# Performance work log

Measured on AMD Instinct MI355X. Metric: run time of the kernel, lower is better.

The kernel has to match this reference:

```python
import jax, jax.numpy as jnp
import numpy as np

PARTICLE_RADIUS = 0.025
RADIUS_SCALE = 1.5
EXTENT = 6.0 * RADIUS_SCALE * PARTICLE_RADIUS   # 0.225
RADIUS = 0.5 * EXTENT                           # 0.1125 search radius
N_FLUID, N_WALL, K = 16000, 8000, 64
KS = 4  # kernel size per axis


def _radius_neighbors(pin, pout, radius, k, exclude_self=False):
    n = pout.shape[0]
    idx = np.zeros((n, k), np.int32)
    mask = np.zeros((n, k), bool)
    r2 = radius * radius
    for s in range(0, n, 2048):
        q = pout[s:s + 2048]
        d2 = ((q[:, None, :] - pin[None, :, :]) ** 2).sum(-1)
        within = d2 < r2
        if exclude_self:
            within &= d2 > 1e-18
        for i in range(q.shape[0]):
            js = np.flatnonzero(within[i])[:k]
            idx[s + i, :js.size] = js
            mask[s + i, :js.size] = True
    return idx, mask


def setup_inputs():
    rng = np.random.RandomState(0)
    L = (N_FLUID / 6700.0) ** (1.0 / 3.0)  # box side -> ~40 nbrs in RADIUS
    fluid_pos = (rng.rand(N_FLUID, 3) * L).astype(np.float32)
    wall_pos = np.stack([rng.rand(N_WALL) * L, -0.3 * rng.rand(N_WALL), rng.rand(N_WALL) * L], -1).astype(np.float32)
    fluid_vel = (0.5 * rng.randn(N_FLUID, 3)).astype(np.float32)
    nv = rng.randn(N_WALL, 3)
    wall_normal_vec = (nv / np.linalg.norm(nv, axis=1, keepdims=True)).astype(np.float32)
    nbr_wf, mask_wf = _radius_neighbors(wall_pos, fluid_pos, RADIUS, K)
    nbr_ff, mask_ff = _radius_neighbors(fluid_pos, fluid_pos, RADIUS, K, exclude_self=True)
    def cw(ci, co):
        return (rng.randn(KS, KS, KS, ci, co) / np.sqrt(ci * KS ** 3)).astype(np.float32)
    def dw(ci, co):
        return (rng.randn(ci, co) / np.sqrt(ci)).astype(np.float32)
    def bias(co):
        return (0.01 * rng.randn(co)).astype(np.float32)
    inp = dict(fluid_pos=fluid_pos, wall_pos=wall_pos, fluid_vel=fluid_vel, wall_normal_vec=wall_normal_vec,
               nbr_wf=nbr_wf, mask_wf=mask_wf, nbr_ff=nbr_ff, mask_ff=mask_ff,
               W_wall1=cw(3, 32), b_wall1=bias(32), W_fluid1=cw(3, 32), b_fluid1=bias(32),
               W_d1=dw(3, 32), b_d1=bias(32),
               W_c2=cw(96, 64), b_c2=bias(64), W_d2=dw(96, 64), b_d2=bias(64),
               W_c3=cw(64, 64), b_c3=bias(64), W_d3=dw(64, 64), b_d3=bias(64),
               W_c4=cw(64, 3), b_c4=bias(3), W_d4=dw(64, 3), b_d4=bias(3))
    return {k_: jnp.asarray(v) for k_, v in inp.items()}


def _ball_to_cube(p):
    """Volume-preserving ball->cylinder->cube map (Open3D coordinate_mapping)."""
    eps = 1e-12
    x, y, z = p[..., 0], p[..., 1], p[..., 2]
    sq = x * x + y * y + z * z
    norm = jnp.sqrt(jnp.maximum(sq, eps))
    rho = jnp.sqrt(jnp.maximum(x * x + y * y, eps))
    top = 1.25 * z * z > x * x + y * y
    s_top = jnp.sqrt(3.0 * norm / (norm + jnp.abs(z)))
    xs = jnp.where(top, x * s_top, x * norm / rho)
    ys = jnp.where(top, y * s_top, y * norm / rho)
    zs = jnp.where(top, jnp.sign(z) * norm, 1.5 * z)
    degen = sq < eps
    xs = jnp.where(degen, 0.0, xs)
    ys = jnp.where(degen, 0.0, ys)
    zs = jnp.where(degen, 0.0, zs)
    # cylinder -> cube: area-preserving disc->square on (x, y)
    rxy = jnp.sqrt(jnp.maximum(xs * xs + ys * ys, eps))
    use_x = jnp.abs(ys) <= jnp.abs(xs)
    dx = jnp.where(use_x & (jnp.abs(xs) > eps), xs, 1.0)
    dy = jnp.where((~use_x) & (jnp.abs(ys) > eps), ys, 1.0)
    c = 4.0 / jnp.pi
    xc = jnp.where(use_x, jnp.sign(xs) * rxy, jnp.sign(ys) * rxy * c * jnp.arctan(xs / dy))
    yc = jnp.where(use_x, jnp.sign(xs) * rxy * c * jnp.arctan(ys / dx), jnp.sign(ys) * rxy)
    deg2 = (xs * xs + ys * ys) < eps
    xc = jnp.where(deg2, 0.0, xc)
    yc = jnp.where(deg2, 0.0, yc)
    return jnp.stack([xc, yc, zs], -1)


def _cconv(feat, pos_in, pos_out, nbr, mask, W, b):
    """ContinuousConv: trilinear kernel interp, poly6 window, normalize=False."""
    n, k = nbr.shape
    cin, cout = W.shape[3], W.shape[4]
    d = (pos_in[nbr] - pos_out[:, None, :]) / RADIUS          # [n,k,3] in unit ball
    d = jnp.where(mask[..., None], d, 0.0)
    r2 = jnp.sum(d * d, -1)
    win = jnp.clip((1.0 - r2) ** 3, 0.0, 1.0)                  # poly6 window
    u = _ball_to_cube(d)                                       # [-1,1]^3
    c = jnp.clip((u * 0.5 + 0.5) * (KS - 1), 0.0, KS - 1.0)   # align_corners coords
    i0 = jnp.clip(jnp.floor(c), 0.0, KS - 2.0)
    f = c - i0
    i0 = i0.astype(jnp.int32)
    feats = feat[nbr] * jnp.where(mask, win, 0.0)[..., None]   # [n,k,cin]
    A = jnp.zeros((n, KS ** 3, cin), feat.dtype)               # per-cell accumulators
    rows = jnp.arange(n)[:, None]
    for cx in (0, 1):
        wx = f[..., 0] if cx else 1.0 - f[..., 0]
        for cy in (0, 1):
            wy = f[..., 1] if cy else 1.0 - f[..., 1]
            for cz in (0, 1):
                wz = f[..., 2] if cz else 1.0 - f[..., 2]
                cell = ((i0[..., 0] + cx) * KS + (i0[..., 1] + cy)) * KS + (i0[..., 2] + cz)
                A = A.at[rows, cell].add((wx * wy * wz)[..., None] * feats)
    return jnp.einsum('nfc,fcd->nd', A, W.reshape(KS ** 3, cin, cout)) + b


def _forward(fluid_pos, wall_pos, fluid_vel, wall_normal_vec, nbr_wf, mask_wf, nbr_ff, mask_ff,
             W_wall1, b_wall1, W_fluid1, b_fluid1, W_d1, b_d1, W_c2, b_c2, W_d2, b_d2,
             W_c3, b_c3, W_d3, b_d3, W_c4, b_c4, W_d4, b_d4):
    wall_1 = jax.nn.relu(_cconv(wall_normal_vec, wall_pos, fluid_pos, nbr_wf, mask_wf, W_wall1, b_wall1))
    fluid_1 = jax.nn.relu(_cconv(fluid_vel, fluid_pos, fluid_pos, nbr_ff, mask_ff, W_fluid1, b_fluid1))
    dense_1 = fluid_vel @ W_d1 + b_d1
    out_1 = jnp.concatenate([wall_1, fluid_1, dense_1], -1)    # [N,96]
    out_2 = jax.nn.relu(_cconv(out_1, fluid_pos, fluid_pos, nbr_ff, mask_ff, W_c2, b_c2) + out_1 @ W_d2 + b_d2)
    out_3 = jax.nn.relu(out_2 + _cconv(out_2, fluid_pos, fluid_pos, nbr_ff, mask_ff, W_c3, b_c3) + out_2 @ W_d3 + b_d3)
    return _cconv(out_3, fluid_pos, fluid_pos, nbr_ff, mask_ff, W_c4, b_c4) + out_3 @ W_d4 + b_d4


def reference(fluid_pos, wall_pos, fluid_vel, wall_normal_vec, nbr_wf, mask_wf, nbr_ff, mask_ff,
              W_wall1, b_wall1, W_fluid1, b_fluid1, W_d1, b_d1, W_c2, b_c2, W_d2, b_d2,
              W_c3, b_c3, W_d3, b_d3, W_c4, b_c4, W_d4, b_d4):
    return _forward(fluid_pos, wall_pos, fluid_vel, wall_normal_vec, nbr_wf, mask_wf, nbr_ff, mask_ff,
                    W_wall1, b_wall1, W_fluid1, b_fluid1, W_d1, b_d1, W_c2, b_c2, W_d2, b_d2,
                    W_c3, b_c3, W_d3, b_d3, W_c4, b_c4, W_d4, b_d4)
```

## Files before the change

### kernel.cpp

```cpp
#include <hip/hip_runtime.h>
#include <hip/hip_bf16.h>


#define M_FLUID 16000
#define KNBR 64

typedef __attribute__((ext_vector_type(8))) short bf16x8;
typedef __attribute__((ext_vector_type(4))) float f32x4;
typedef __attribute__((ext_vector_type(4))) unsigned short u16x4;

__device__ __forceinline__ ushort f2bf(float f) {
    __hip_bfloat16 h = __float2bfloat16(f);
    return *(ushort*)&h;
}

__device__ __forceinline__ float sgnf(float v) {
    return (v > 0.f) ? 1.f : ((v < 0.f) ? -1.f : 0.f);
}

__device__ __forceinline__ void ball_to_cube(float x, float y, float z,
                                             float& xc, float& yc, float& zc) {
    const float eps = 1e-12f;
    float sq  = x*x + y*y + z*z;
    float nrm = sqrtf(fmaxf(sq, eps));
    float rho = sqrtf(fmaxf(x*x + y*y, eps));
    bool  top = (1.25f*z*z > x*x + y*y);
    float s_top = sqrtf(3.0f*nrm/(nrm + fabsf(z)));
    float xs = top ? x*s_top : x*nrm/rho;
    float ys = top ? y*s_top : y*nrm/rho;
    float zs = top ? sgnf(z)*nrm : 1.5f*z;
    if (sq < eps) { xs = 0.f; ys = 0.f; zs = 0.f; }
    float rxy = sqrtf(fmaxf(xs*xs + ys*ys, eps));
    bool use_x = fabsf(ys) <= fabsf(xs);
    float dx = (use_x && fabsf(xs) > eps) ? xs : 1.0f;
    float dy = (!use_x && fabsf(ys) > eps) ? ys : 1.0f;
    const float c4pi = 1.2732395447351628f;
    float xc_, yc_;
    if (use_x) {
        xc_ = sgnf(xs)*rxy;
        yc_ = sgnf(xs)*rxy*c4pi*atanf(ys/dx);
    } else {
        xc_ = sgnf(ys)*rxy*c4pi*atanf(xs/dy);
        yc_ = sgnf(ys)*rxy;
    }
    if (xs*xs + ys*ys < eps) { xc_ = 0.f; yc_ = 0.f; }
    xc = xc_; yc = yc_; zc = zs;
}

__global__ void geom_dual_kernel(const float* __restrict__ fluid_pos,
                                 const float* __restrict__ wall_pos,
                                 const int*  __restrict__ nbrF,
                                 const int*  __restrict__ nbrW,
                                 float4* __restrict__ gFf, int* __restrict__ gIf,
                                 float4* __restrict__ gFw, int* __restrict__ gIw,
                                 int M) {
    int t = blockIdx.x * blockDim.x + threadIdx.x;
    if (t >= M * KNBR) return;
    const float* pos_in; const int* nbr; float4* geomF; int* geomI; int excl_self;
    if (blockIdx.y == 0) { pos_in = fluid_pos; nbr = nbrF; geomF = gFf; geomI = gIf; excl_self = 1; }
    else                 { pos_in = wall_pos;  nbr = nbrW; geomF = gFw; geomI = gIw; excl_self = 0; }
    int n = t >> 6;
    int k = t & 63;
    int j = nbr[t];
    float px = fluid_pos[n*3+0], py = fluid_pos[n*3+1], pz = fluid_pos[n*3+2];
    float qx = pos_in[(size_t)j*3+0], qy = pos_in[(size_t)j*3+1], qz = pos_in[(size_t)j*3+2];
    float dx = qx - px, dy = qy - py, dz = qz - pz;

    bool valid;
    if (k == 0) {
#pragma clang fp contract(off)
        float d2f = dx*dx + dy*dy;
        d2f = d2f + dz*dz;
        double d2 = (double)d2f;
        const double RADIUS_D = 0.5*(6.0*1.5*0.025);
        valid = d2 < RADIUS_D*RADIUS_D;
        if (excl_self) valid = valid && (d2 > 1e-18);
    } else {
        valid = (j != 0);
    }

    const float Rf = (float)(0.5*(6.0*1.5*0.025));
    float ux = dx / Rf, uy = dy / Rf, uz = dz / Rf;
    float r2 = ux*ux + uy*uy; r2 += uz*uz;
    float w1 = 1.f - r2;
    float win = fminf(fmaxf(w1*w1*w1, 0.f), 1.f);

    float bx, by, bz;
    ball_to_cube(ux, uy, uz, bx, by, bz);
    float cx = fminf(fmaxf((bx*0.5f + 0.5f)*3.f, 0.f), 3.f);
    float cy = fminf(fmaxf((by*0.5f + 0.5f)*3.f, 0.f), 3.f);
    float cz = fminf(fmaxf((bz*0.5f + 0.5f)*3.f, 0.f), 3.f);
    float ix = fminf(fmaxf(floorf(cx), 0.f), 2.f);
    float iy = fminf(fmaxf(floorf(cy), 0.f), 2.f);
    float iz = fminf(fmaxf(floorf(cz), 0.f), 2.f);
    float fx = cx - ix, fy = cy - iy, fz = cz - iz;
    int cell = ((int)ix*4 + (int)iy)*4 + (int)iz;

    geomF[t] = make_float4(valid ? win : 0.f, fx, fy, fz);
    geomI[t] = cell;
}

template<int CIN>
__global__ __launch_bounds__(64) void abuild_s_kernel(
        const float* __restrict__ feat,
        const int*   __restrict__ nbr,
        const float4* __restrict__ geomF,
        const int*   __restrict__ geomI,
        const float* __restrict__ dense,
        ushort* __restrict__ A,
        int m0, int m1, int Ktot) {
    constexpr int SP = 72;
    constexpr int NT = CIN / 16;
    __shared__ ushort S[64*SP];
    __shared__ ushort FW[CIN*SP];
    int l = threadIdx.x;
    int n = m0 + blockIdx.x;
    if (n >= m1) return;

    {
        uint4 z = make_uint4(0,0,0,0);
        uint4* Sv = (uint4*)S;
#pragma unroll
        for (int i = 0; i < (64*SP*2)/(16*64); ++i)
            Sv[l + 64*i] = z;
    }
    size_t t = (size_t)n * KNBR + l;
    float4 g = geomF[t];
    int cell = geomI[t];
    int j = nbr[t];
    {
        float win = g.x;
        float x1 = g.y, y1 = g.z, z1 = g.w;
        float x0 = 1.f-x1, y0 = 1.f-y1, z0 = 1.f-z1;
        float w00 = y0*z0*win, w01 = y0*z1*win, w10 = y1*z0*win, w11 = y1*z1*win;
        ushort* Sc = S + cell*SP + l;
        Sc[0*SP]  = f2bf(x0*w00);
        Sc[1*SP]  = f2bf(x0*w01);
        Sc[4*SP]  = f2bf(x0*w10);
        Sc[5*SP]  = f2bf(x0*w11);
        Sc[16*SP] = f2bf(x1*w00);
        Sc[17*SP] = f2bf(x1*w01);
        Sc[20*SP] = f2bf(x1*w10);
        Sc[21*SP] = f2bf(x1*w11);
    }
    {
        const float* frow = feat + (size_t)j * CIN;
#pragma unroll
        for (int c4 = 0; c4 < CIN; c4 += 4) {
            float4 v = *(const float4*)(frow + c4);
            FW[(c4+0)*SP + l] = f2bf(v.x);
            FW[(c4+1)*SP + l] = f2bf(v.y);
            FW[(c4+2)*SP + l] = f2bf(v.z);
            FW[(c4+3)*SP + l] = f2bf(v.w);
        }
    }
    int lm = l & 15, koct = l >> 4;
    f32x4 acc[4][NT];
#pragma unroll
    for (int mt = 0; mt < 4; ++mt)
#pragma unroll
        for (int nt = 0; nt < NT; ++nt)
            acc[mt][nt] = (f32x4){0.f, 0.f, 0.f, 0.f};
#pragma unroll
    for (int ks = 0; ks < 2; ++ks) {
        bf16x8 sf[4];
#pragma unroll
        for (int mt = 0; mt < 4; ++mt)
            sf[mt] = *(const bf16x8*)&S[(mt*16 + lm)*SP + ks*32 + koct*8];
#pragma unroll
        for (int nt = 0; nt < NT; ++nt) {
            bf16x8 ff = *(const bf16x8*)&FW[(nt*16 + lm)*SP + ks*32 + koct*8];
#pragma unroll
            for (int mt = 0; mt < 4; ++mt)
                acc[mt][nt] = __builtin_amdgcn_mfma_f32_16x16x32_bf16(
                                  sf[mt], ff, acc[mt][nt], 0, 0, 0);
        }
    }
    ushort* AT = FW;
#pragma unroll
    for (int nt = 0; nt < NT; ++nt)
#pragma unroll
        for (int mt = 0; mt < 4; ++mt) {
            u16x4 pk;
            pk.x = f2bf(acc[mt][nt][0]);
            pk.y = f2bf(acc[mt][nt][1]);
            pk.z = f2bf(acc[mt][nt][2]);
            pk.w = f2bf(acc[mt][nt][3]);
            *(u16x4*)&AT[(nt*16 + lm)*SP + mt*16 + koct*4] = pk;
        }
    ushort* Arow = A + (size_t)(n - m0) * Ktot;
#pragma unroll
    for (int it = 0; it < CIN/8; ++it) {
        int i = l + 64*it;
        int ch = i >> 3, cc = (i & 7) * 8;
        uint4 v = *(const uint4*)&AT[ch*SP + cc];
        *(uint4*)&Arow[(ch << 6) + cc] = v;
    }
#pragma unroll
    for (int c0 = 0; c0 < CIN; c0 += 64) {
        int ch = c0 + l;
        if (ch < CIN) Arow[64*CIN + ch] = f2bf(dense[(size_t)n*CIN + ch]);
    }
}

__global__ __launch_bounds__(64) void abuild_s3_dual_kernel(
        const float* __restrict__ featW, const float* __restrict__ featF,
        const int*   __restrict__ nbrW,  const int*   __restrict__ nbrF,
        const float4* __restrict__ gFw,  const int* __restrict__ gIw,
        const float4* __restrict__ gFf,  const int* __restrict__ gIf,
        ushort* __restrict__ A0, ushort* __restrict__ A1, int M) {
    constexpr int SP = 72;
    constexpr int Ktot = 192;
    __shared__ ushort S[64*SP];
    __shared__ ushort FW[16*SP];
    const float* feat; const int* nbr; const float4* geomF; const int* geomI; ushort* A;
    if (blockIdx.y == 0) { feat = featW; nbr = nbrW; geomF = gFw; geomI = gIw; A = A0; }
    else                 { feat = featF; nbr = nbrF; geomF = gFf; geomI = gIf; A = A1; }
    int l = threadIdx.x;
    int n = blockIdx.x;
    if (n >= M) return;

    {
        uint4 z = make_uint4(0,0,0,0);
        uint4* Sv = (uint4*)S;
#pragma unroll
        for (int i = 0; i < 9; ++i) Sv[l + 64*i] = z;
        uint4* Fv = (uint4*)FW;
#pragma unroll
        for (int i = 0; i < 3; ++i) {
            int idx = l + 64*i;
            if (idx < (16*SP*2)/16) Fv[idx] = z;
        }
    }
    size_t t = (size_t)n * KNBR + l;
    float4 g = geomF[t];
    int cell = geomI[t];
    int j = nbr[t];
    {
        float win = g.x;
        float x1 = g.y, y1 = g.z, z1 = g.w;
        float x0 = 1.f-x1, y0 = 1.f-y1, z0 = 1.f-z1;
        float w00 = y0*z0*win, w01 = y0*z1*win, w10 = y1*z0*win, w11 = y1*z1*win;
        ushort* Sc = S + cell*SP + l;
        Sc[0*SP]  = f2bf(x0*w00);
        Sc[1*SP]  = f2bf(x0*w01);
        Sc[4*SP]  = f2bf(x0*w10);
        Sc[5*SP]  = f2bf(x0*w11);
        Sc[16*SP] = f2bf(x1*w00);
        Sc[17*SP] = f2bf(x1*w01);
        Sc[20*SP] = f2bf(x1*w10);
        Sc[21*SP] = f2bf(x1*w11);
    }
    {
        const float* fr = feat + (size_t)j * 3;
        FW[0*SP + l] = f2bf(fr[0]);
        FW[1*SP + l] = f2bf(fr[1]);
        FW[2*SP + l] = f2bf(fr[2]);
    }
    int lm = l & 15, koct = l >> 4;
    f32x4 acc[4];
#pragma unroll
    for (int mt = 0; mt < 4; ++mt) acc[mt] = (f32x4){0.f,0.f,0.f,0.f};
#pragma unroll
    for (int ks = 0; ks < 2; ++ks) {
        bf16x8 ff = *(const bf16x8*)&FW[lm*SP + ks*32 + koct*8];
#pragma unroll
        for (int mt = 0; mt < 4; ++mt) {
            bf16x8 sf = *(const bf16x8*)&S[(mt*16 + lm)*SP + ks*32 + koct*8];
            acc[mt] = __builtin_amdgcn_mfma_f32_16x16x32_bf16(sf, ff, acc[mt], 0, 0, 0);
        }
    }
    ushort* AT = FW;
    if (lm < 3) {
#pragma unroll
        for (int mt = 0; mt < 4; ++mt) {
            u16x4 pk;
            pk.x = f2bf(acc[mt][0]);
            pk.y = f2bf(acc[mt][1]);
            pk.z = f2bf(acc[mt][2]);
            pk.w = f2bf(acc[mt][3]);
            *(u16x4*)&AT[lm*SP + mt*16 + koct*4] = pk;
        }
    }
    ushort* Arow = A + (size_t)n * Ktot;
    if (l < 24) {
        int ch = l >> 3, cc = (l & 7) * 8;
        *(uint4*)&Arow[ch*64 + cc] = *(const uint4*)&AT[ch*SP + cc];
    }
}

__global__ void dense1_kernel(const float* __restrict__ vel,
                              const float* __restrict__ Wd,
                              const float* __restrict__ bd,
                              float* __restrict__ out1, int M) {
    int t = blockIdx.x * blockDim.x + threadIdx.x;
    if (t >= M*32) return;
    int n = t >> 5, c = t & 31;
    float v = bd[c] + vel[n*3+0]*Wd[c] + vel[n*3+1]*Wd[32+c] + vel[n*3+2]*Wd[64+c];
    out1[(size_t)n*96 + 64 + c] = v;
}

__device__ __forceinline__ void wprep_one(const float* Wc, int Kc,
                                          const float* Wd, int N,
                                          ushort* Wt, int Ktot, int t) {
    int nn = t / Ktot, k = t - nn * Ktot;
    float v;
    if (k < Kc) {
        int cinl = Kc >> 6;
        int ch = k >> 6, cl = k & 63;
        v = Wc[(size_t)(cl*cinl + ch)*N + nn];
    } else {
        v = Wd[(size_t)(k-Kc)*N + nn];
    }
    Wt[(size_t)nn*Ktot + k] = f2bf(v);
}

__global__ void wprep_all_kernel(
        const float* __restrict__ W_wall1, const float* __restrict__ W_fluid1,
        const float* __restrict__ W_c2, const float* __restrict__ W_d2,
        const float* __restrict__ W_c3, const float* __restrict__ W_d3,
        const float* __restrict__ W_c4,
        ushort* __restrict__ Wt1a, ushort* __restrict__ Wt1b,
        ushort* __restrict__ Wt2, ushort* __restrict__ Wt3,
        ushort* __restrict__ Wt4) {
    int t = blockIdx.x * 256 + threadIdx.x;
    const int s0 = 32*192, s1 = s0 + 32*192, s2 = s1 + 64*6240,
              s3 = s2 + 64*4160, s4 = s3 + 192*64;
    if (t < s0) {
        wprep_one(W_wall1, 192, nullptr, 32, Wt1a, 192, t);
    } else if (t < s1) {
        wprep_one(W_fluid1, 192, nullptr, 32, Wt1b, 192, t - s0);
    } else if (t < s2) {
        wprep_one(W_c2, 6144, W_d2, 64, Wt2, 6240, t - s1);
    } else if (t < s3) {
        wprep_one(W_c3, 4096, W_d3, 64, Wt3, 4160, t - s2);
    } else if (t < s4) {
        int u = t - s3;
        int row = u >> 6, ch = u & 63;
        int cell = row / 3, c = row - cell*3;
        Wt4[row*64 + ch] = f2bf(W_c4[(cell*64 + ch)*3 + c]);
    }
}

__global__ __launch_bounds__(256) void gemm_l1_kernel(
        const ushort* __restrict__ A0, const ushort* __restrict__ A1,
        const ushort* __restrict__ Wt0, const ushort* __restrict__ Wt1,
        const float* __restrict__ b0, const float* __restrict__ b1,
        float* __restrict__ out1, int M) {
    constexpr int Ktot = 192, nks = 6, NCT = 2;
    const ushort* A;  const ushort* Wt; const float* bias; int ocol;
    if (blockIdx.y == 0) { A = A0; Wt = Wt0; bias = b0; ocol = 0; }
    else                 { A = A1; Wt = Wt1; bias = b1; ocol = 32; }
    int tid = threadIdx.x;
    int w = tid >> 6, l = tid & 63;
    int lm = l & 15, koct = l >> 4;
    int mb = blockIdx.x;

    const ushort* Arow = A + (size_t)(mb*64 + w*16 + lm) * Ktot + koct*8;
    const ushort* Wrow = Wt + (size_t)lm * Ktot + koct*8;

    f32x4 acc[NCT];
#pragma unroll
    for (int ct = 0; ct < NCT; ++ct) acc[ct] = (f32x4){0.f,0.f,0.f,0.f};

    bf16x8 ac = *(const bf16x8*)(Arow);
    bf16x8 bc[NCT];
#pragma unroll
    for (int ct = 0; ct < NCT; ++ct)
        bc[ct] = *(const bf16x8*)(Wrow + (size_t)ct*16*Ktot);
#pragma unroll
    for (int ks = 0; ks < nks; ++ks) {
        bf16x8 an = {};
        bf16x8 bn[NCT] = {};
        if (ks + 1 < nks) {
            int k0 = (ks + 1) * 32;
            an = *(const bf16x8*)(Arow + k0);
#pragma unroll
            for (int ct = 0; ct < NCT; ++ct)
                bn[ct] = *(const bf16x8*)(Wrow + (size_t)ct*16*Ktot + k0);
        }
#pragma unroll
        for (int ct = 0; ct < NCT; ++ct)
            acc[ct] = __builtin_amdgcn_mfma_f32_16x16x32_bf16(ac, bc[ct], acc[ct], 0, 0, 0);
        ac = an;
#pragma unroll
        for (int ct = 0; ct < NCT; ++ct) bc[ct] = bn[ct];
    }

    int rbase = mb*64 + w*16 + koct*4;
#pragma unroll
    for (int ct = 0; ct < NCT; ++ct) {
        int col = ct*16 + lm;
        float bb = bias[col];
#pragma unroll
        for (int r = 0; r < 4; ++r) {
            float v = fmaxf(acc[ct][r] + bb, 0.f);
            out1[(size_t)(rbase + r)*96 + ocol + col] = v;
        }
    }
}

__global__ __launch_bounds__(256) void gemm7_kernel(
        const ushort* __restrict__ A, int Ktot,
        const ushort* __restrict__ Wt,
        float* __restrict__ Cpart, int rows, int nks, int KS) {
    constexpr int N = 64;
    constexpr int SP = 40;
    __shared__ ushort Ash[2][128][SP];
    __shared__ ushort Bsh[2][64][SP];
    int tid = threadIdx.x;
    int w = tid >> 6, l = tid & 63;
    int lm = l & 15, koct = l >> 4;
    int mb = blockIdx.x;
    int per = (nks + KS - 1) / KS;
    int ksa = blockIdx.y * per;
    int ksb = ksa + per; if (ksb > nks) ksb = nks;
    int nk = ksb - ksa;

    f32x4 acc[2][4];
#pragma unroll
    for (int fi = 0; fi < 2; ++fi)
#pragma unroll
        for (int nt = 0; nt < 4; ++nt) acc[fi][nt] = (f32x4){0.f,0.f,0.f,0.f};

    int rS  = tid >> 2;
    int kb4 = tid & 3;
    int rA0 = mb*128 + rS;       if (rA0 >= rows) rA0 = rows - 1;
    int rA1 = mb*128 + rS + 64;  if (rA1 >= rows) rA1 = rows - 1;

    bf16x8 ra0, ra1, rb;
    auto load_regs = [&](int ks) {
        int kk = ks*32 + kb4*8;
        ra0 = *(const bf16x8*)&A[(size_t)rA0*Ktot + kk];
        ra1 = *(const bf16x8*)&A[(size_t)rA1*Ktot + kk];
        rb  = *(const bf16x8*)&Wt[(size_t)rS*Ktot + kk];
    };
    auto store_lds = [&](int buf) {
        *(bf16x8*)&Ash[buf][rS][kb4*8]      = ra0;
        *(bf16x8*)&Ash[buf][rS + 64][kb4*8] = ra1;
        *(bf16x8*)&Bsh[buf][rS][kb4*8]      = rb;
    };

    if (nk > 0) {
        load_regs(ksa);
        store_lds(0);
        __syncthreads();
        for (int i = 0; i < nk; ++i) {
            int buf = i & 1;
            bool nxt = (i + 1 < nk);
            if (nxt) load_regs(ksa + i + 1);
            bf16x8 a0 = *(const bf16x8*)&Ash[buf][w*32 + lm][koct*8];
            bf16x8 a1 = *(const bf16x8*)&Ash[buf][w*32 + 16 + lm][koct*8];
#pragma unroll
            for (int nt = 0; nt < 4; ++nt) {
                bf16x8 b = *(const bf16x8*)&Bsh[buf][nt*16 + lm][koct*8];
                acc[0][nt] = __builtin_amdgcn_mfma_f32_16x16x32_bf16(a0, b, acc[0][nt], 0, 0, 0);
                acc[1][nt] = __builtin_amdgcn_mfma_f32_16x16x32_bf16(a1, b, acc[1][nt], 0, 0, 0);
            }
            if (nxt) {
                store_lds(buf ^ 1);
                __syncthreads();
            }
        }
    }

    float* Cp = Cpart + ((size_t)blockIdx.y * rows + mb*128 + w*32) * N;
    int gr0 = mb*128 + w*32;
#pragma unroll
    for (int fi = 0; fi < 2; ++fi)
#pragma unroll
        for (int nt = 0; nt < 4; ++nt)
#pragma unroll
            for (int r = 0; r < 4; ++r) {
                int row = fi*16 + koct*4 + r;
                if (gr0 + row < rows)
                    Cp[row * N + nt*16 + lm] = acc[fi][nt][r];
            }
}

__global__ __launch_bounds__(256) void reduce_kernel(
        const float* __restrict__ Cpart, int rows, int N, int KS,
        const float* __restrict__ b1, const float* __restrict__ b2,
        const float* __restrict__ res,
        float* __restrict__ out, int ostride, int ocol, int m_base, int relu,
        ushort* __restrict__ outb) {
    int idx = blockIdx.x * 256 + threadIdx.x;
    int nq = N >> 2;
    if (idx >= rows * nq) return;
    int row = idx / nq;
    int c4 = (idx - row * nq) * 4;
    size_t slab = (size_t)rows * N;
    const float* p = Cpart + (size_t)row * N + c4;
    float s0 = 0.f, s1 = 0.f, s2 = 0.f, s3 = 0.f;
    for (int k = 0; k < KS; ++k) {
        float4 v = *(const float4*)(p + slab * k);
        s0 += v.x; s1 += v.y; s2 += v.z; s3 += v.w;
    }
    s0 += b1[c4+0]; s1 += b1[c4+1]; s2 += b1[c4+2]; s3 += b1[c4+3];
    if (b2) { s0 += b2[c4+0]; s1 += b2[c4+1]; s2 += b2[c4+2]; s3 += b2[c4+3]; }
    if (res) {
        const float* rr = res + (size_t)(m_base + row) * 64 + c4;
        s0 += rr[0]; s1 += rr[1]; s2 += rr[2]; s3 += rr[3];
    }
    if (relu) {
        s0 = fmaxf(s0, 0.f); s1 = fmaxf(s1, 0.f);
        s2 = fmaxf(s2, 0.f); s3 = fmaxf(s3, 0.f);
    }
    float* o = out + (size_t)(m_base + row) * ostride + ocol + c4;
    *(float4*)o = make_float4(s0, s1, s2, s3);
    if (outb) {
        u16x4 pk;
        pk.x = f2bf(s0); pk.y = f2bf(s1); pk.z = f2bf(s2); pk.w = f2bf(s3);
        *(u16x4*)&outb[(size_t)(m_base + row) * 64 + c4] = pk;
    }
}

__global__ __launch_bounds__(256) void g4_mfma_kernel(
        const ushort* __restrict__ out3b,
        const ushort* __restrict__ Wt4,
        float* __restrict__ G, int M) {
    constexpr int SP = 72;
    __shared__ ushort Bsh[192*SP];
    int tid = threadIdx.x;
    for (int u = tid; u < 192*8; u += 256) {
        int row = u >> 3, seg = u & 7;
        *(bf16x8*)&Bsh[row*SP + seg*8] = *(const bf16x8*)&Wt4[row*64 + seg*8];
    }
    __syncthreads();
    int w = tid >> 6, l = tid & 63;
    int lm = l & 15, koct = l >> 4;
    int row0 = blockIdx.x*64 + w*16;
    const ushort* Arow = out3b + (size_t)(row0 + lm)*64 + koct*8;
    bf16x8 a0 = *(const bf16x8*)(Arow);
    bf16x8 a1 = *(const bf16x8*)(Arow + 32);
    f32x4 acc[12];
#pragma unroll
    for (int nt = 0; nt < 12; ++nt) acc[nt] = (f32x4){0.f,0.f,0.f,0.f};
#pragma unroll
    for (int nt = 0; nt < 12; ++nt) {
        bf16x8 b = *(const bf16x8*)&Bsh[(nt*16 + lm)*SP + koct*8];
        acc[nt] = __builtin_amdgcn_mfma_f32_16x16x32_bf16(a0, b, acc[nt], 0, 0, 0);
    }
#pragma unroll
    for (int nt = 0; nt < 12; ++nt) {
        bf16x8 b = *(const bf16x8*)&Bsh[(nt*16 + lm)*SP + 32 + koct*8];
        acc[nt] = __builtin_amdgcn_mfma_f32_16x16x32_bf16(a1, b, acc[nt], 0, 0, 0);
    }
#pragma unroll
    for (int nt = 0; nt < 12; ++nt)
#pragma unroll
        for (int r = 0; r < 4; ++r)
            G[(size_t)(row0 + koct*4 + r)*192 + nt*16 + lm] = acc[nt][r];
}

__global__ __launch_bounds__(256) void l4_scatter_kernel(
        const float* __restrict__ G,
        const float4* __restrict__ geomF,
        const int*   __restrict__ geomI,
        const int*   __restrict__ nbr,
        const float* __restrict__ out3,
        const float* __restrict__ Wd4,
        const float* __restrict__ b_c4, const float* __restrict__ b_d4,
        float* __restrict__ out, int M) {
    __shared__ float Wsh[192];
    int tid = threadIdx.x;
    if (tid < 192) Wsh[tid] = Wd4[tid];
    __syncthreads();
    int wv = tid >> 6, l = tid & 63;
    int n = blockIdx.x*4 + wv;
    if (n >= M) return;
    size_t t = (size_t)n * KNBR + l;
    float4 g = geomF[t];
    int cell = geomI[t];
    int j = nbr[t];
    float a0 = 0.f, a1 = 0.f, a2 = 0.f;
    float win = g.x;
    if (win > 0.f) {
        float x1 = g.y, y1 = g.z, z1 = g.w;
        float x0 = 1.f-x1, y0 = 1.f-y1, z0 = 1.f-z1;
        float w[8] = {x0*y0*z0, x0*y0*z1, x0*y1*z0, x0*y1*z1,
                      x1*y0*z0, x1*y0*z1, x1*y1*z0, x1*y1*z1};
        const int co[8] = {0,1,4,5,16,17,20,21};
        const float* Gj = G + (size_t)j*192;
#pragma unroll
        for (int i = 0; i < 8; ++i) {
            const float* Gc = Gj + (cell + co[i])*3;
            float ww = win * w[i];
            a0 += ww*Gc[0]; a1 += ww*Gc[1]; a2 += ww*Gc[2];
        }
    }
    {
        float v = out3[(size_t)n*64 + l];
        a0 += v*Wsh[l*3+0]; a1 += v*Wsh[l*3+1]; a2 += v*Wsh[l*3+2];
    }
#pragma unroll
    for (int off = 32; off; off >>= 1) {
        a0 += __shfl_down(a0, off, 64);
        a1 += __shfl_down(a1, off, 64);
        a2 += __shfl_down(a2, off, 64);
    }
    if (l == 0) {
        out[n*3+0] = a0 + b_c4[0] + b_d4[0];
        out[n*3+1] = a1 + b_c4[1] + b_d4[1];
        out[n*3+2] = a2 + b_c4[2] + b_d4[2];
    }
}

extern "C" void kernel_launch(void* const* d_in, const int* in_sizes, int n_in,
                              void* d_out, int out_size, void* d_ws, size_t ws_size,
                              hipStream_t stream) {
    const float* fluid_pos = (const float*)d_in[0];
    const float* wall_pos  = (const float*)d_in[1];
    const float* fluid_vel = (const float*)d_in[2];
    const float* wall_nrm  = (const float*)d_in[3];
    const int*   nbr_wf    = (const int*)d_in[4];
    const int*   nbr_ff    = (const int*)d_in[6];
    const float* W_wall1   = (const float*)d_in[8];
    const float* b_wall1   = (const float*)d_in[9];
    const float* W_fluid1  = (const float*)d_in[10];
    const float* b_fluid1  = (const float*)d_in[11];
    const float* W_d1      = (const float*)d_in[12];
    const float* b_d1      = (const float*)d_in[13];
    const float* W_c2      = (const float*)d_in[14];
    const float* b_c2      = (const float*)d_in[15];
    const float* W_d2      = (const float*)d_in[16];
    const float* b_d2      = (const float*)d_in[17];
    const float* W_c3      = (const float*)d_in[18];
    const float* b_c3      = (const float*)d_in[19];
    const float* W_d3      = (const float*)d_in[20];
    const float* b_d3      = (const float*)d_in[21];
    const float* W_c4      = (const float*)d_in[22];
    const float* b_c4      = (const float*)d_in[23];
    const float* W_d4      = (const float*)d_in[24];
    const float* b_d4      = (const float*)d_in[25];

    const int M = M_FLUID;
    char* ws = (char*)d_ws;
    size_t off = 0;
    auto carve = [&](size_t bytes) {
        char* p = ws + off;
        off = (off + bytes + 255) & ~(size_t)255;
        return p;
    };
    float4* gF_ff = (float4*)carve((size_t)M*KNBR*sizeof(float4));
    int*    gI_ff = (int*)   carve((size_t)M*KNBR*4);
    float4* gF_wf = (float4*)carve((size_t)M*KNBR*sizeof(float4));
    int*    gI_wf = (int*)   carve((size_t)M*KNBR*4);
    float*  out1  = (float*) carve((size_t)M*96*4);
    float*  out2  = (float*) carve((size_t)M*64*4);
    float*  out3  = (float*) carve((size_t)M*64*4);
    ushort* out3b = (ushort*)carve((size_t)M*64*2);
    float*  Gbuf  = (float*) carve((size_t)M*192*4);
    ushort* Wt1a  = (ushort*)carve((size_t)32*192*2);
    ushort* Wt1b  = (ushort*)carve((size_t)32*192*2);
    ushort* Wt2   = (ushort*)carve((size_t)64*6240*2);
    ushort* Wt3   = (ushort*)carve((size_t)64*4160*2);
    ushort* Wt4   = (ushort*)carve((size_t)192*64*2);
    float*  Cpart = (float*) carve((size_t)8*M*64*4);
    ushort* Abuf  = (ushort*)(ws + off);
    size_t availA = (ws_size > off) ? (ws_size - off) : 0;

    auto chunkR = [&](int Ktot) -> int {
        size_t r = availA / ((size_t)Ktot * 2);
        if (r > (size_t)M) r = (size_t)M;
        r &= ~(size_t)127;
        if (r < 128) r = 128;
        return (int)r;
    };

    {
        int total = 2*32*192 + 64*6240 + 64*4160 + 192*64;
        wprep_all_kernel<<<(total + 255)/256, 256, 0, stream>>>(
            W_wall1, W_fluid1, W_c2, W_d2, W_c3, W_d3, W_c4,
            Wt1a, Wt1b, Wt2, Wt3, Wt4);
    }
    {
        int total = M * KNBR, thr = 256;
        geom_dual_kernel<<<dim3((total + thr - 1)/thr, 2), thr, 0, stream>>>(
            fluid_pos, wall_pos, nbr_ff, nbr_wf, gF_ff, gI_ff, gF_wf, gI_wf, M);
    }
    dense1_kernel<<<(M*32 + 255)/256, 256, 0, stream>>>(fluid_vel, W_d1, b_d1, out1, M);

    {
        ushort* A0 = Abuf;
        ushort* A1 = Abuf + (size_t)M*192;
        abuild_s3_dual_kernel<<<dim3(M, 2), 64, 0, stream>>>(
            wall_nrm, fluid_vel, nbr_wf, nbr_ff,
            gF_wf, gI_wf, gF_ff, gI_ff, A0, A1, M);
        gemm_l1_kernel<<<dim3(M/64, 2), 256, 0, stream>>>(
            A0, A1, Wt1a, Wt1b, b_wall1, b_fluid1, out1, M);
    }
    {
        int Ktot = 6240, nks = 195, KS = 8, R = chunkR(Ktot);
        for (int m0 = 0; m0 < M; m0 += R) {
            int rows = (M - m0 < R) ? (M - m0) : R;
            abuild_s_kernel<96><<<rows, 64, 0, stream>>>(
                out1, nbr_ff, gF_ff, gI_ff, out1, Abuf, m0, m0+rows, Ktot);
            gemm7_kernel<<<dim3((rows+127)/128, KS), 256, 0, stream>>>(
                Abuf, Ktot, Wt2, Cpart, rows, nks, KS);
            reduce_kernel<<<(rows*16 + 255)/256, 256, 0, stream>>>(
                Cpart, rows, 64, KS, b_c2, b_d2, nullptr,
                out2, 64, 0, m0, 1, nullptr);
        }
    }
    {
        int Ktot = 4160, nks = 130, KS = 8, R = chunkR(Ktot);
        for (int m0 = 0; m0 < M; m0 += R) {
            int rows = (M - m0 < R) ? (M - m0) : R;
            abuild_s_kernel<64><<<rows, 64, 0, stream>>>(
                out2, nbr_ff, gF_ff, gI_ff, out2, Abuf, m0, m0+rows, Ktot);
            gemm7_kernel<<<dim3((rows+127)/128, KS), 256, 0, stream>>>(
                Abuf, Ktot, Wt3, Cpart, rows, nks, KS);
            reduce_kernel<<<(rows*16 + 255)/256, 256, 0, stream>>>(
                Cpart, rows, 64, KS, b_c3, b_d3, out2,
                out3, 64, 0, m0, 1, out3b);
        }
    }
    g4_mfma_kernel<<<M/64, 256, 0, stream>>>(out3b, Wt4, Gbuf, M);
    l4_scatter_kernel<<<(M+3)/4, 256, 0, stream>>>(
        Gbuf, gF_ff, gI_ff, nbr_ff, out3, W_d4, b_c4, b_d4, (float*)d_out, M);
}
```

Baseline: 386.3 us.

## Software-pipeline A-matrix build and GEMM across chunks in fused launches

Merges the neighbor-feature A-build and the split-K GEMM into one kernel launch whose blocks run either role. Chunk c's A-build now runs concurrently with chunk c-1's GEMM, using double-buffered A storage. The A-build packs four neighbourhoods per 256-thread block and processes channels in two halves to cut shared memory. Cpart is indexed globally so a single reduce runs at the end. The cost is a fixed chunk size of 4000 rows, which assumes the workspace holds two A buffers, plus mixed-role blocks competing for resources.

Result: slower. 433.4 us (+12.2%).

```diff
diff --git a/kernel.cpp b/kernel.cpp
--- a/kernel.cpp
+++ b/kernel.cpp
@@ -101,28 +101,25 @@
 }
 
 template<int CIN>
-__global__ __launch_bounds__(64) void abuild_s_kernel(
-        const float* __restrict__ feat,
-        const int*   __restrict__ nbr,
-        const float4* __restrict__ geomF,
-        const int*   __restrict__ geomI,
-        const float* __restrict__ dense,
-        ushort* __restrict__ A,
+__device__ __forceinline__ void abuild_body(char* smem, int blk,
+        const float* __restrict__ feat, const int* __restrict__ nbr,
+        const float4* __restrict__ geomF, const int* __restrict__ geomI,
+        const float* __restrict__ dense, ushort* __restrict__ A,
         int m0, int m1, int Ktot) {
+    constexpr int H = CIN / 2;
+    constexpr int NTH = H / 16;
     constexpr int SP = 72;
-    constexpr int NT = CIN / 16;
-    __shared__ ushort S[64*SP];
-    __shared__ ushort FW[CIN*SP];
-    int l = threadIdx.x;
-    int n = m0 + blockIdx.x;
+    int w = threadIdx.x >> 6, l = threadIdx.x & 63;
+    ushort* S  = (ushort*)(smem + (size_t)w * ((64 + H) * SP * 2));
+    ushort* FW = S + 64*SP;
+    int n = m0 + blk*4 + w;
     if (n >= m1) return;
 
     {
         uint4 z = make_uint4(0,0,0,0);
         uint4* Sv = (uint4*)S;
 #pragma unroll
-        for (int i = 0; i < (64*SP*2)/(16*64); ++i)
-            Sv[l + 64*i] = z;
+        for (int i = 0; i < 9; ++i) Sv[l + 64*i] = z;
     }
     size_t t = (size_t)n * KNBR + l;
     float4 g = geomF[t];
@@ -143,63 +140,158 @@
         Sc[20*SP] = f2bf(x1*w10);
         Sc[21*SP] = f2bf(x1*w11);
     }
-    {
-        const float* frow = feat + (size_t)j * CIN;
-#pragma unroll
-        for (int c4 = 0; c4 < CIN; c4 += 4) {
-            float4 v = *(const float4*)(frow + c4);
+    int lm = l & 15, koct = l >> 4;
+    const float* frow = feat + (size_t)j * CIN;
+    ushort* Arow = A + (size_t)(n - m0) * Ktot;
+#pragma unroll
+    for (int h = 0; h < 2; ++h) {
+#pragma unroll
+        for (int c4 = 0; c4 < H; c4 += 4) {
+            float4 v = *(const float4*)(frow + h*H + c4);
             FW[(c4+0)*SP + l] = f2bf(v.x);
             FW[(c4+1)*SP + l] = f2bf(v.y);
             FW[(c4+2)*SP + l] = f2bf(v.z);
             FW[(c4+3)*SP + l] = f2bf(v.w);
         }
-    }
-    int lm = l & 15, koct = l >> 4;
-    f32x4 acc[4][NT];
-#pragma unroll
-    for (int mt = 0; mt < 4; ++mt)
-#pragma unroll
-        for (int nt = 0; nt < NT; ++nt)
-            acc[mt][nt] = (f32x4){0.f, 0.f, 0.f, 0.f};
-#pragma unroll
-    for (int ks = 0; ks < 2; ++ks) {
-        bf16x8 sf[4];
+        f32x4 acc[4][NTH];
 #pragma unroll
         for (int mt = 0; mt < 4; ++mt)
-            sf[mt] = *(const bf16x8*)&S[(mt*16 + lm)*SP + ks*32 + koct*8];
-#pragma unroll
-        for (int nt = 0; nt < NT; ++nt) {
-            bf16x8 ff = *(const bf16x8*)&FW[(nt*16 + lm)*SP + ks*32 + koct*8];
+#pragma unroll
+            for (int nt = 0; nt < NTH; ++nt)
+                acc[mt][nt] = (f32x4){0.f,0.f,0.f,0.f};
+#pragma unroll
+        for (int ks = 0; ks < 2; ++ks) {
+            bf16x8 sf[4];
 #pragma unroll
             for (int mt = 0; mt < 4; ++mt)
-                acc[mt][nt] = __builtin_amdgcn_mfma_f32_16x16x32_bf16(
-                                  sf[mt], ff, acc[mt][nt], 0, 0, 0);
-        }
-    }
-    ushort* AT = FW;
-#pragma unroll
-    for (int nt = 0; nt < NT; ++nt)
-#pragma unroll
-        for (int mt = 0; mt < 4; ++mt) {
-            u16x4 pk;
-            pk.x = f2bf(acc[mt][nt][0]);
-            pk.y = f2bf(acc[mt][nt][1]);
-            pk.z = f2bf(acc[mt][nt][2]);
-            pk.w = f2bf(acc[mt][nt][3]);
-            *(u16x4*)&AT[(nt*16 + lm)*SP + mt*16 + koct*4] = pk;
-        }
-    ushort* Arow = A + (size_t)(n - m0) * Ktot;
-#pragma unroll
-    for (int it = 0; it < CIN/8; ++it) {
-        int i = l + 64*it;
-        int ch = i >> 3, cc = (i & 7) * 8;
-        uint4 v = *(const uint4*)&AT[ch*SP + cc];
-        *(uint4*)&Arow[(ch << 6) + cc] = v;
+                sf[mt] = *(const bf16x8*)&S[(mt*16 + lm)*SP + ks*32 + koct*8];
+#pragma unroll
+            for (int nt = 0; nt < NTH; ++nt) {
+                bf16x8 ff = *(const bf16x8*)&FW[(nt*16 + lm)*SP + ks*32 + koct*8];
+#pragma unroll
+                for (int mt = 0; mt < 4; ++mt)
+                    acc[mt][nt] = __builtin_amdgcn_mfma_f32_16x16x32_bf16(
+                                      sf[mt], ff, acc[mt][nt], 0, 0, 0);
+            }
+        }
+        ushort* AT = FW;
+#pragma unroll
+        for (int nt = 0; nt < NTH; ++nt)
+#pragma unroll
+            for (int mt = 0; mt < 4; ++mt) {
+                u16x4 pk;
+                pk.x = f2bf(acc[mt][nt][0]);
+                pk.y = f2bf(acc[mt][nt][1]);
+                pk.z = f2bf(acc[mt][nt][2]);
+                pk.w = f2bf(acc[mt][nt][3]);
+                *(u16x4*)&AT[(nt*16 + lm)*SP + mt*16 + koct*4] = pk;
+            }
+#pragma unroll
+        for (int it = 0; it < H/8; ++it) {
+            int i = l + 64*it;
+            int ch = i >> 3, cc = (i & 7) * 8;
+            *(uint4*)&Arow[(h*H + ch)*64 + cc] = *(const uint4*)&AT[ch*SP + cc];
+        }
     }
 #pragma unroll
     for (int c0 = 0; c0 < CIN; c0 += 64) {
         int ch = c0 + l;
         if (ch < CIN) Arow[64*CIN + ch] = f2bf(dense[(size_t)n*CIN + ch]);
+    }
+}
+
+__device__ __forceinline__ void gemm_body(char* smem, int gblk,
+        const ushort* __restrict__ A, int Ktot, const ushort* __restrict__ Wt,
+        float* __restrict__ Cpart, int rows, int gm0, int nks, int KS, int Mtot) {
+    constexpr int SP = 40;
+    ushort* Ash = (ushort*)smem;
+    ushort* Bsh = Ash + 2*128*SP;
+    int tid = threadIdx.x;
+    int w = tid >> 6, l = tid & 63;
+    int lm = l & 15, koct = l >> 4;
+    int mb = gblk / KS;
+    int ksy = gblk - mb*KS;
+    int per = (nks + KS - 1) / KS;
+    int ksa = ksy * per;
+    int ksb = ksa + per; if (ksb > nks) ksb = nks;
+    int nk = ksb - ksa;
+
+    f32x4 acc[2][4];
+#pragma unroll
+    for (int fi = 0; fi < 2; ++fi)
+#pragma unroll
+        for (int nt = 0; nt < 4; ++nt) acc[fi][nt] = (f32x4){0.f,0.f,0.f,0.f};
+
+    int rS  = tid >> 2;
+    int kb4 = tid & 3;
+    int rA0 = mb*128 + rS;       if (rA0 >= rows) rA0 = rows - 1;
+    int rA1 = mb*128 + rS + 64;  if (rA1 >= rows) rA1 = rows - 1;
+
+    bf16x8 ra0, ra1, rb;
+    auto load_regs = [&](int ks) {
+        int kk = ks*32 + kb4*8;
+        ra0 = *(const bf16x8*)&A[(size_t)rA0*Ktot + kk];
+        ra1 = *(const bf16x8*)&A[(size_t)rA1*Ktot + kk];
+        rb  = *(const bf16x8*)&Wt[(size_t)rS*Ktot + kk];
+    };
+    auto store_lds = [&](int buf) {
+        *(bf16x8*)&Ash[(buf*128 + rS)*SP + kb4*8]      = ra0;
+        *(bf16x8*)&Ash[(buf*128 + rS + 64)*SP + kb4*8] = ra1;
+        *(bf16x8*)&Bsh[(buf*64 + rS)*SP + kb4*8]       = rb;
+    };
+
+    if (nk > 0) {
+        load_regs(ksa);
+        store_lds(0);
+        __syncthreads();
+        for (int i = 0; i < nk; ++i) {
+            int buf = i & 1;
+            bool nxt = (i + 1 < nk);
+            if (nxt) load_regs(ksa + i + 1);
+            bf16x8 a0 = *(const bf16x8*)&Ash[(buf*128 + w*32 + lm)*SP + koct*8];
+            bf16x8 a1 = *(const bf16x8*)&Ash[(buf*128 + w*32 + 16 + lm)*SP + koct*8];
+#pragma unroll
+            for (int nt = 0; nt < 4; ++nt) {
+                bf16x8 b = *(const bf16x8*)&Bsh[(buf*64 + nt*16 + lm)*SP + koct*8];
+                acc[0][nt] = __builtin_amdgcn_mfma_f32_16x16x32_bf16(a0, b, acc[0][nt], 0, 0, 0);
+                acc[1][nt] = __builtin_amdgcn_mfma_f32_16x16x32_bf16(a1, b, acc[1][nt], 0, 0, 0);
+            }
+            if (nxt) {
+                store_lds(buf ^ 1);
+                __syncthreads();
+            }
+        }
+    }
+
+    float* Cp = Cpart + ((size_t)ksy * Mtot + gm0 + mb*128 + w*32) * 64;
+    int gr0 = mb*128 + w*32;
+#pragma unroll
+    for (int fi = 0; fi < 2; ++fi)
+#pragma unroll
+        for (int nt = 0; nt < 4; ++nt)
+#pragma unroll
+            for (int r = 0; r < 4; ++r) {
+                int row = fi*16 + koct*4 + r;
+                if (gr0 + row < rows)
+                    Cp[row * 64 + nt*16 + lm] = acc[fi][nt][r];
+            }
+}
+
+template<int CIN>
+__global__ __launch_bounds__(256) void fused_stage_kernel(
+        const ushort* __restrict__ Ag, int Ktot, const ushort* __restrict__ Wt,
+        float* __restrict__ Cpart, int grows, int ggm0, int nks, int KS,
+        int Mtot, int G_gemm,
+        const float* __restrict__ feat, const int* __restrict__ nbr,
+        const float4* __restrict__ geomF, const int* __restrict__ geomI,
+        const float* __restrict__ dense, ushort* __restrict__ Aa,
+        int am0, int am1) {
+    extern __shared__ char smem[];
+    if ((int)blockIdx.x < G_gemm) {
+        gemm_body(smem, blockIdx.x, Ag, Ktot, Wt, Cpart, grows, ggm0, nks, KS, Mtot);
+    } else {
+        abuild_body<CIN>(smem, blockIdx.x - G_gemm, feat, nbr, geomF, geomI,
+                         dense, Aa, am0, am1, Ktot);
     }
 }
 
@@ -398,84 +490,6 @@
             out1[(size_t)(rbase + r)*96 + ocol + col] = v;
         }
     }
-}
-
-__global__ __launch_bounds__(256) void gemm7_kernel(
-        const ushort* __restrict__ A, int Ktot,
-        const ushort* __restrict__ Wt,
-        float* __restrict__ Cpart, int rows, int nks, int KS) {
-    constexpr int N = 64;
-    constexpr int SP = 40;
-    __shared__ ushort Ash[2][128][SP];
-    __shared__ ushort Bsh[2][64][SP];
-    int tid = threadIdx.x;
-    int w = tid >> 6, l = tid & 63;
-    int lm = l & 15, koct = l >> 4;
-    int mb = blockIdx.x;
-    int per = (nks + KS - 1) / KS;
-    int ksa = blockIdx.y * per;
-    int ksb = ksa + per; if (ksb > nks) ksb = nks;
-    int nk = ksb - ksa;
-
-    f32x4 acc[2][4];
-#pragma unroll
-    for (int fi = 0; fi < 2; ++fi)
-#pragma unroll
-        for (int nt = 0; nt < 4; ++nt) acc[fi][nt] = (f32x4){0.f,0.f,0.f,0.f};
-
-    int rS  = tid >> 2;
-    int kb4 = tid & 3;
-    int rA0 = mb*128 + rS;       if (rA0 >= rows) rA0 = rows - 1;
-    int rA1 = mb*128 + rS + 64;  if (rA1 >= rows) rA1 = rows - 1;
-
-    bf16x8 ra0, ra1, rb;
-    auto load_regs = [&](int ks) {
-        int kk = ks*32 + kb4*8;
-        ra0 = *(const bf16x8*)&A[(size_t)rA0*Ktot + kk];
-        ra1 = *(const bf16x8*)&A[(size_t)rA1*Ktot + kk];
-        rb  = *(const bf16x8*)&Wt[(size_t)rS*Ktot + kk];
-    };
-    auto store_lds = [&](int buf) {
-        *(bf16x8*)&Ash[buf][rS][kb4*8]      = ra0;
-        *(bf16x8*)&Ash[buf][rS + 64][kb4*8] = ra1;
-        *(bf16x8*)&Bsh[buf][rS][kb4*8]      = rb;
-    };
-
-    if (nk > 0) {
-        load_regs(ksa);
-        store_lds(0);
-        __syncthreads();
-        for (int i = 0; i < nk; ++i) {
-            int buf = i & 1;
-            bool nxt = (i + 1 < nk);
-            if (nxt) load_regs(ksa + i + 1);
-            bf16x8 a0 = *(const bf16x8*)&Ash[buf][w*32 + lm][koct*8];
-            bf16x8 a1 = *(const bf16x8*)&Ash[buf][w*32 + 16 + lm][koct*8];
-#pragma unroll
-            for (int nt = 0; nt < 4; ++nt) {
-                bf16x8 b = *(const bf16x8*)&Bsh[buf][nt*16 + lm][koct*8];
-                acc[0][nt] = __builtin_amdgcn_mfma_f32_16x16x32_bf16(a0, b, acc[0][nt], 0, 0, 0);
-                acc[1][nt] = __builtin_amdgcn_mfma_f32_16x16x32_bf16(a1, b, acc[1][nt], 0, 0, 0);
-            }
-            if (nxt) {
-                store_lds(buf ^ 1);
-                __syncthreads();
-            }
-        }
-    }
-
-    float* Cp = Cpart + ((size_t)blockIdx.y * rows + mb*128 + w*32) * N;
-    int gr0 = mb*128 + w*32;
-#pragma unroll
-    for (int fi = 0; fi < 2; ++fi)
-#pragma unroll
-        for (int nt = 0; nt < 4; ++nt)
-#pragma unroll
-            for (int r = 0; r < 4; ++r) {
-                int row = fi*16 + koct*4 + r;
-                if (gr0 + row < rows)
-                    Cp[row * N + nt*16 + lm] = acc[fi][nt][r];
-            }
 }
 
 __global__ __launch_bounds__(256) void reduce_kernel(
@@ -658,15 +672,6 @@
     ushort* Wt4   = (ushort*)carve((size_t)192*64*2);
     float*  Cpart = (float*) carve((size_t)8*M*64*4);
     ushort* Abuf  = (ushort*)(ws + off);
-    size_t availA = (ws_size > off) ? (ws_size - off) : 0;
-
-    auto chunkR = [&](int Ktot) -> int {
-        size_t r = availA / ((size_t)Ktot * 2);
-        if (r > (size_t)M) r = (size_t)M;
-        r &= ~(size_t)127;
-        if (r < 128) r = 128;
-        return (int)r;
-    };
 
     {
         int total = 2*32*192 + 64*6240 + 64*4160 + 192*64;
@@ -691,30 +696,36 @@
             A0, A1, Wt1a, Wt1b, b_wall1, b_fluid1, out1, M);
     }
     {
-        int Ktot = 6240, nks = 195, KS = 8, R = chunkR(Ktot);
-        for (int m0 = 0; m0 < M; m0 += R) {
-            int rows = (M - m0 < R) ? (M - m0) : R;
-            abuild_s_kernel<96><<<rows, 64, 0, stream>>>(
-                out1, nbr_ff, gF_ff, gI_ff, out1, Abuf, m0, m0+rows, Ktot);
-            gemm7_kernel<<<dim3((rows+127)/128, KS), 256, 0, stream>>>(
-                Abuf, Ktot, Wt2, Cpart, rows, nks, KS);
-            reduce_kernel<<<(rows*16 + 255)/256, 256, 0, stream>>>(
-                Cpart, rows, 64, KS, b_c2, b_d2, nullptr,
-                out2, 64, 0, m0, 1, nullptr);
-        }
-    }
-    {
-        int Ktot = 4160, nks = 130, KS = 8, R = chunkR(Ktot);
-        for (int m0 = 0; m0 < M; m0 += R) {
-            int rows = (M - m0 < R) ? (M - m0) : R;
-            abuild_s_kernel<64><<<rows, 64, 0, stream>>>(
-                out2, nbr_ff, gF_ff, gI_ff, out2, Abuf, m0, m0+rows, Ktot);
-            gemm7_kernel<<<dim3((rows+127)/128, KS), 256, 0, stream>>>(
-                Abuf, Ktot, Wt3, Cpart, rows, nks, KS);
-            reduce_kernel<<<(rows*16 + 255)/256, 256, 0, stream>>>(
-                Cpart, rows, 64, KS, b_c3, b_d3, out2,
-                out3, 64, 0, m0, 1, out3b);
-        }
+        const int Ktot = 6240, nks = 195, KS = 8, R = 4000, NCH = 4;
+        ushort* Ab[2] = {Abuf, Abuf + (size_t)R*Ktot};
+        size_t dyn = (size_t)4*(64+48)*72*2;
+        int mt = (R + 127)/128;
+        for (int c = 0; c <= NCH; ++c) {
+            int G_g = (c > 0)   ? mt*KS : 0;
+            int G_a = (c < NCH) ? R/4   : 0;
+            int gm0 = (c-1)*R, am0 = c*R;
+            fused_stage_kernel<96><<<G_g + G_a, 256, dyn, stream>>>(
+                Ab[(c-1) & 1], Ktot, Wt2, Cpart, R, gm0, nks, KS, M, G_g,
+                out1, nbr_ff, gF_ff, gI_ff, out1, Ab[c & 1], am0, am0 + R);
+        }
+        reduce_kernel<<<(M*16 + 255)/256, 256, 0, stream>>>(
+            Cpart, M, 64, KS, b_c2, b_d2, nullptr, out2, 64, 0, 0, 1, nullptr);
+    }
+    {
+        const int Ktot = 4160, nks = 130, KS = 8, R = 4000, NCH = 4;
+        ushort* Ab[2] = {Abuf, Abuf + (size_t)R*Ktot};
+        size_t dyn = (size_t)4*(64+32)*72*2;
+        int mt = (R + 127)/128;
+        for (int c = 0; c <= NCH; ++c) {
+            int G_g = (c > 0)   ? mt*KS : 0;
+            int G_a = (c < NCH) ? R/4   : 0;
+            int gm0 = (c-1)*R, am0 = c*R;
+            fused_stage_kernel<64><<<G_g + G_a, 256, dyn, stream>>>(
+                Ab[(c-1) & 1], Ktot, Wt3, Cpart, R, gm0, nks, KS, M, G_g,
+                out2, nbr_ff, gF_ff, gI_ff, out2, Ab[c & 1], am0, am0 + R);
+        }
+        reduce_kernel<<<(M*16 + 255)/256, 256, 0, stream>>>(
+            Cpart, M, 64, KS, b_c3, b_d3, out2, out3, 64, 0, 0, 1, out3b);
     }
     g4_mfma_kernel<<<M/64, 256, 0, stream>>>(out3b, Wt4, Gbuf, M);
     l4_scatter_kernel<<<(M+3)/4, 256, 0, stream>>>(
```
